# Optimization experiments

Measured on AMD Instinct MI355X. Metric: run time of the kernel, lower is better.

The kernel has to match this reference:

```python
import jax, jax.numpy as jnp
import numpy as np

BOHR = 1.8897261258369282  # au.BOHR length conversion constant


def setup_inputs() -> dict:
    key = jax.random.key(0)
    k0, k1, k2, k3, k4, k5, k6 = jax.random.split(key, 7)
    B, N, NK = 2, 4096, 4096
    coords = jax.random.normal(k0, (B, N, 3), jnp.float32) * 5.0
    q = jax.random.normal(k1, (B, N), jnp.float32)
    cell_inv = jax.random.normal(k2, (3, 3), jnp.float32) * 0.05  # inverse cell matrix
    kvec = jax.random.normal(k3, (NK, 3), jnp.float32)            # reciprocal lattice vectors
    expfac = jax.random.uniform(k4, (NK,), jnp.float32)           # exp(-k^2/4b^2)/k^2 factors
    volume = jax.random.uniform(k5, (1,), jnp.float32) + 100.0    # cell volume (positive)
    bewald = jax.random.uniform(k6, (1,), jnp.float32)            # Ewald splitting parameter
    return {"coords": coords, "q": q, "cell_inv": cell_inv, "kvec": kvec,
            "expfac": expfac, "volume": volume, "bewald": bewald}


def reference(coords, q, cell_inv, kvec, expfac, volume, bewald):
    # fractional coordinates: s[b,n,i] = cell_inv[i,j] coords[b,n,j]
    s = jnp.einsum('ij,bnj->bni', cell_inv, coords)
    # phase theta[b,n,k] = 2*pi * (kvec[k] . s[b,n]);  ks = i*theta in the original
    theta = (2.0 * jnp.pi) * jnp.einsum('kd,bnd->bnk', kvec, s)
    c = jnp.cos(theta)
    sn = jnp.sin(theta)
    # structure factor Sm[b,k] = sum_n q[b,n] * exp(i*theta[b,n,k])
    s_re = jnp.einsum('bn,bnk->bk', q, c)
    s_im = jnp.einsum('bn,bnk->bk', q, sn)
    # Re( expfac * Sm * exp(-i*theta) ) = expfac * (Sre*cos + Sim*sin)
    recip = (jnp.einsum('k,bk,bnk->bn', expfac, s_re, c)
             + jnp.einsum('k,bk,bnk->bn', expfac, s_im, sn))
    phi = recip * (BOHR / (jnp.pi * volume[0])) \
          - q * (2.0 * bewald[0] * BOHR / jnp.pi ** 0.5)
    return (0.5 * q * phi, phi)
```

## Files before the change

kernel.cpp:

```cpp
#include <hip/hip_runtime.h>


constexpr int B  = 2;
constexpr int N  = 4096;
constexpr int NK = 4096;
constexpr int TPB = 256;
constexpr int NSPLIT1 = 16;
constexpr int NSPLIT2 = 16;

constexpr int KT_OFF  = 0;
constexpr int SRE_OFF = NK * 3;
constexpr int SIM_OFF = SRE_OFF + B * NK;
constexpr int REC_OFF = SIM_OFF + B * NK;
constexpr int WS_FLOATS = REC_OFF + B * N;

__global__ __launch_bounds__(256) void prep_kt(const float* __restrict__ kvec,
                                               const float* __restrict__ cinv,
                                               float* __restrict__ ws) {
    int k = blockIdx.x * TPB + threadIdx.x;
    if (k >= NK) return;
    float k0 = kvec[k * 3 + 0], k1 = kvec[k * 3 + 1], k2 = kvec[k * 3 + 2];
    ws[KT_OFF + k * 3 + 0] = fmaf(k0, cinv[0], fmaf(k1, cinv[3], k2 * cinv[6]));
    ws[KT_OFF + k * 3 + 1] = fmaf(k0, cinv[1], fmaf(k1, cinv[4], k2 * cinv[7]));
    ws[KT_OFF + k * 3 + 2] = fmaf(k0, cinv[2], fmaf(k1, cinv[5], k2 * cinv[8]));
}

__global__ __launch_bounds__(256) void sf_kernel(const float* __restrict__ coords,
                                                 const float* __restrict__ q,
                                                 float* __restrict__ ws) {
    const int b = blockIdx.z;
    const int k = blockIdx.x * TPB + threadIdx.x;
    const int chunk = N / NSPLIT1;
    const int n0 = blockIdx.y * chunk;
    const float* cb = coords + (size_t)b * N * 3;
    const float* qb = q + (size_t)b * N;

    const float kt0 = ws[KT_OFF + k * 3 + 0];
    const float kt1 = ws[KT_OFF + k * 3 + 1];
    const float kt2 = ws[KT_OFF + k * 3 + 2];

    __shared__ float sc[TPB * 3];
    __shared__ float sq[TPB];

    float sre0 = 0.f, sre1 = 0.f, sim0 = 0.f, sim1 = 0.f;

    for (int t0 = 0; t0 < chunk; t0 += TPB) {
        const int base = n0 + t0;
        __syncthreads();
        sq[threadIdx.x] = qb[base + threadIdx.x];
#pragma unroll
        for (int j = 0; j < 3; ++j)
            sc[j * TPB + threadIdx.x] = cb[(size_t)base * 3 + j * TPB + threadIdx.x];
        __syncthreads();
#pragma unroll 8
        for (int i = 0; i < TPB; i += 2) {
            {
                float x = sc[3 * i + 0], y = sc[3 * i + 1], z = sc[3 * i + 2];
                float rev = fmaf(kt0, x, fmaf(kt1, y, kt2 * z));
                float r = rev - floorf(rev);
                float sn = __builtin_amdgcn_sinf(r);
                float cs = __builtin_amdgcn_cosf(r);
                float qv = sq[i];
                sre0 = fmaf(qv, cs, sre0);
                sim0 = fmaf(qv, sn, sim0);
            }
            {
                float x = sc[3 * i + 3], y = sc[3 * i + 4], z = sc[3 * i + 5];
                float rev = fmaf(kt0, x, fmaf(kt1, y, kt2 * z));
                float r = rev - floorf(rev);
                float sn = __builtin_amdgcn_sinf(r);
                float cs = __builtin_amdgcn_cosf(r);
                float qv = sq[i + 1];
                sre1 = fmaf(qv, cs, sre1);
                sim1 = fmaf(qv, sn, sim1);
            }
        }
    }
    atomicAdd(&ws[SRE_OFF + b * NK + k], sre0 + sre1);
    atomicAdd(&ws[SIM_OFF + b * NK + k], sim0 + sim1);
}

__global__ __launch_bounds__(256) void recip_kernel(const float* __restrict__ coords,
                                                    const float* __restrict__ expfac,
                                                    float* __restrict__ ws) {
    const int b = blockIdx.z;
    const int n = blockIdx.x * TPB + threadIdx.x;
    const int chunk = NK / NSPLIT2;
    const int k0 = blockIdx.y * chunk;

    const float* cp = coords + ((size_t)b * N + n) * 3;
    const float x = cp[0], y = cp[1], z = cp[2];

    __shared__ float skt[TPB * 3];
    __shared__ float sre[TPB];
    __shared__ float sim[TPB];

    float acc0 = 0.f, acc1 = 0.f;

    for (int t0 = 0; t0 < chunk; t0 += TPB) {
        const int kb = k0 + t0;
        const int t = threadIdx.x;
        __syncthreads();
        {
            float ef = expfac[kb + t];
            sre[t] = ef * ws[SRE_OFF + b * NK + kb + t];
            sim[t] = ef * ws[SIM_OFF + b * NK + kb + t];
#pragma unroll
            for (int j = 0; j < 3; ++j)
                skt[j * TPB + t] = ws[KT_OFF + (size_t)kb * 3 + j * TPB + t];
        }
        __syncthreads();
#pragma unroll 8
        for (int i = 0; i < TPB; i += 2) {
            {
                float kt0 = skt[3 * i + 0], kt1 = skt[3 * i + 1], kt2 = skt[3 * i + 2];
                float rev = fmaf(kt0, x, fmaf(kt1, y, kt2 * z));
                float r = rev - floorf(rev);
                float sn = __builtin_amdgcn_sinf(r);
                float cs = __builtin_amdgcn_cosf(r);
                acc0 = fmaf(sre[i], cs, fmaf(sim[i], sn, acc0));
            }
            {
                float kt0 = skt[3 * i + 3], kt1 = skt[3 * i + 4], kt2 = skt[3 * i + 5];
                float rev = fmaf(kt0, x, fmaf(kt1, y, kt2 * z));
                float r = rev - floorf(rev);
                float sn = __builtin_amdgcn_sinf(r);
                float cs = __builtin_amdgcn_cosf(r);
                acc1 = fmaf(sre[i + 1], cs, fmaf(sim[i + 1], sn, acc1));
            }
        }
    }
    atomicAdd(&ws[REC_OFF + b * N + n], acc0 + acc1);
}

__global__ __launch_bounds__(256) void final_kernel(const float* __restrict__ q,
                                                    const float* __restrict__ volume,
                                                    const float* __restrict__ bewald,
                                                    const float* __restrict__ ws,
                                                    float* __restrict__ out) {
    int i = blockIdx.x * TPB + threadIdx.x;
    if (i >= B * N) return;
    const float BOHRf = 1.8897261258369282f;
    const float PIf = 3.14159265358979323846f;
    const float inv_sqrt_pi = 0.5641895835477563f;
    float scale = BOHRf / (PIf * volume[0]);
    float self = 2.0f * bewald[0] * BOHRf * inv_sqrt_pi;
    float qv = q[i];
    float phi = ws[REC_OFF + i] * scale - qv * self;
    out[i] = 0.5f * qv * phi;
    out[B * N + i] = phi;
}

extern "C" void kernel_launch(void* const* d_in, const int* in_sizes, int n_in,
                              void* d_out, int out_size, void* d_ws, size_t ws_size,
                              hipStream_t stream) {
    const float* coords = (const float*)d_in[0];
    const float* q      = (const float*)d_in[1];
    const float* cinv   = (const float*)d_in[2];
    const float* kvec   = (const float*)d_in[3];
    const float* expfac = (const float*)d_in[4];
    const float* volume = (const float*)d_in[5];
    const float* bewald = (const float*)d_in[6];
    float* out = (float*)d_out;
    float* ws  = (float*)d_ws;

    hipMemsetAsync(ws + SRE_OFF, 0, (size_t)(WS_FLOATS - SRE_OFF) * sizeof(float), stream);

    prep_kt<<<dim3(NK / TPB), dim3(TPB), 0, stream>>>(kvec, cinv, ws);
    sf_kernel<<<dim3(NK / TPB, NSPLIT1, B), dim3(TPB), 0, stream>>>(coords, q, ws);
    recip_kernel<<<dim3(N / TPB, NSPLIT2, B), dim3(TPB), 0, stream>>>(coords, expfac, ws);
    final_kernel<<<dim3((B * N + TPB - 1) / TPB), dim3(TPB), 0, stream>>>(q, volume, bewald, ws, out);
}
```

Measured before the change: 93.22 us.

## Pack atoms and k-vectors as float4, pre-scale structure factors, split finer

```diff
diff --git a/kernel.cpp b/kernel.cpp
--- a/kernel.cpp
+++ b/kernel.cpp
@@ -1,136 +1,117 @@
 #include <hip/hip_runtime.h>
 
 
-constexpr int B  = 2;
-constexpr int N  = 4096;
-constexpr int NK = 4096;
+constexpr int B   = 2;
+constexpr int N   = 4096;
+constexpr int NK  = 4096;
 constexpr int TPB = 256;
-constexpr int NSPLIT1 = 16;
-constexpr int NSPLIT2 = 16;
+constexpr int NS1 = 64;
+constexpr int NS2 = 64;
+constexpr int TILE1 = N / NS1;
+constexpr int TILE2 = NK / NS2;
 
-constexpr int KT_OFF  = 0;
-constexpr int SRE_OFF = NK * 3;
-constexpr int SIM_OFF = SRE_OFF + B * NK;
-constexpr int REC_OFF = SIM_OFF + B * NK;
-constexpr int WS_FLOATS = REC_OFF + B * N;
+constexpr int KT4 = 0;
+constexpr int AT4 = KT4 + NK * 4;
+constexpr int SRE = AT4 + B * N * 4;
+constexpr int SIM = SRE + B * NK;
+constexpr int REC = SIM + B * NK;
+constexpr int SP  = REC + B * N;
+constexpr int ZERO_FLOATS = 2 * B * NK + B * N;
 
-__global__ __launch_bounds__(256) void prep_kt(const float* __restrict__ kvec,
-                                               const float* __restrict__ cinv,
-                                               float* __restrict__ ws) {
-    int k = blockIdx.x * TPB + threadIdx.x;
-    if (k >= NK) return;
-    float k0 = kvec[k * 3 + 0], k1 = kvec[k * 3 + 1], k2 = kvec[k * 3 + 2];
-    ws[KT_OFF + k * 3 + 0] = fmaf(k0, cinv[0], fmaf(k1, cinv[3], k2 * cinv[6]));
-    ws[KT_OFF + k * 3 + 1] = fmaf(k0, cinv[1], fmaf(k1, cinv[4], k2 * cinv[7]));
-    ws[KT_OFF + k * 3 + 2] = fmaf(k0, cinv[2], fmaf(k1, cinv[5], k2 * cinv[8]));
+__global__ __launch_bounds__(256) void prep_kernel(const float* __restrict__ coords,
+                                                   const float* __restrict__ q,
+                                                   const float* __restrict__ cinv,
+                                                   const float* __restrict__ kvec,
+                                                   float* __restrict__ ws) {
+    int i = blockIdx.x * TPB + threadIdx.x;
+    if (i < NK) {
+        float k0 = kvec[i * 3 + 0], k1 = kvec[i * 3 + 1], k2 = kvec[i * 3 + 2];
+        ws[KT4 + 4 * i + 0] = fmaf(k0, cinv[0], fmaf(k1, cinv[3], k2 * cinv[6]));
+        ws[KT4 + 4 * i + 1] = fmaf(k0, cinv[1], fmaf(k1, cinv[4], k2 * cinv[7]));
+        ws[KT4 + 4 * i + 2] = fmaf(k0, cinv[2], fmaf(k1, cinv[5], k2 * cinv[8]));
+        ws[KT4 + 4 * i + 3] = 0.f;
+    }
+    if (i < B * N) {
+        ws[AT4 + 4 * i + 0] = coords[3 * i + 0];
+        ws[AT4 + 4 * i + 1] = coords[3 * i + 1];
+        ws[AT4 + 4 * i + 2] = coords[3 * i + 2];
+        ws[AT4 + 4 * i + 3] = q[i];
+    }
 }
 
-__global__ __launch_bounds__(256) void sf_kernel(const float* __restrict__ coords,
-                                                 const float* __restrict__ q,
-                                                 float* __restrict__ ws) {
+__global__ __launch_bounds__(256) void sf_kernel(float* __restrict__ ws) {
     const int b = blockIdx.z;
     const int k = blockIdx.x * TPB + threadIdx.x;
-    const int chunk = N / NSPLIT1;
-    const int n0 = blockIdx.y * chunk;
-    const float* cb = coords + (size_t)b * N * 3;
-    const float* qb = q + (size_t)b * N;
+    const int n0 = blockIdx.y * TILE1;
 
-    const float kt0 = ws[KT_OFF + k * 3 + 0];
-    const float kt1 = ws[KT_OFF + k * 3 + 1];
-    const float kt2 = ws[KT_OFF + k * 3 + 2];
+    const float4 kt = *(const float4*)&ws[KT4 + 4 * k];
 
-    __shared__ float sc[TPB * 3];
-    __shared__ float sq[TPB];
+    __shared__ float sat[TILE1 * 4];
+    sat[threadIdx.x] = ws[AT4 + (size_t)(b * N + n0) * 4 + threadIdx.x];
+    __syncthreads();
 
+    const float4* a4 = (const float4*)sat;
     float sre0 = 0.f, sre1 = 0.f, sim0 = 0.f, sim1 = 0.f;
-
-    for (int t0 = 0; t0 < chunk; t0 += TPB) {
-        const int base = n0 + t0;
-        __syncthreads();
-        sq[threadIdx.x] = qb[base + threadIdx.x];
 #pragma unroll
-        for (int j = 0; j < 3; ++j)
-            sc[j * TPB + threadIdx.x] = cb[(size_t)base * 3 + j * TPB + threadIdx.x];
-        __syncthreads();
-#pragma unroll 8
-        for (int i = 0; i < TPB; i += 2) {
-            {
-                float x = sc[3 * i + 0], y = sc[3 * i + 1], z = sc[3 * i + 2];
-                float rev = fmaf(kt0, x, fmaf(kt1, y, kt2 * z));
-                float r = rev - floorf(rev);
-                float sn = __builtin_amdgcn_sinf(r);
-                float cs = __builtin_amdgcn_cosf(r);
-                float qv = sq[i];
-                sre0 = fmaf(qv, cs, sre0);
-                sim0 = fmaf(qv, sn, sim0);
-            }
-            {
-                float x = sc[3 * i + 3], y = sc[3 * i + 4], z = sc[3 * i + 5];
-                float rev = fmaf(kt0, x, fmaf(kt1, y, kt2 * z));
-                float r = rev - floorf(rev);
-                float sn = __builtin_amdgcn_sinf(r);
-                float cs = __builtin_amdgcn_cosf(r);
-                float qv = sq[i + 1];
-                sre1 = fmaf(qv, cs, sre1);
-                sim1 = fmaf(qv, sn, sim1);
-            }
-        }
+    for (int i = 0; i < TILE1; i += 2) {
+        float4 a = a4[i];
+        float4 c = a4[i + 1];
+        float r0 = fmaf(kt.x, a.x, fmaf(kt.y, a.y, kt.z * a.z));
+        r0 -= floorf(r0);
+        float r1 = fmaf(kt.x, c.x, fmaf(kt.y, c.y, kt.z * c.z));
+        r1 -= floorf(r1);
+        sre0 = fmaf(a.w, __builtin_amdgcn_cosf(r0), sre0);
+        sim0 = fmaf(a.w, __builtin_amdgcn_sinf(r0), sim0);
+        sre1 = fmaf(c.w, __builtin_amdgcn_cosf(r1), sre1);
+        sim1 = fmaf(c.w, __builtin_amdgcn_sinf(r1), sim1);
     }
-    atomicAdd(&ws[SRE_OFF + b * NK + k], sre0 + sre1);
-    atomicAdd(&ws[SIM_OFF + b * NK + k], sim0 + sim1);
+    atomicAdd(&ws[SRE + b * NK + k], sre0 + sre1);
+    atomicAdd(&ws[SIM + b * NK + k], sim0 + sim1);
 }
 
-__global__ __launch_bounds__(256) void recip_kernel(const float* __restrict__ coords,
-                                                    const float* __restrict__ expfac,
-                                                    float* __restrict__ ws) {
+__global__ __launch_bounds__(256) void pack_kernel(const float* __restrict__ expfac,
+                                                   float* __restrict__ ws) {
+    int i = blockIdx.x * TPB + threadIdx.x;
+    if (i >= B * NK) return;
+    int k = i & (NK - 1);
+    float ef = expfac[k];
+    ws[SP + 2 * i + 0] = ef * ws[SRE + i];
+    ws[SP + 2 * i + 1] = ef * ws[SIM + i];
+}
+
+__global__ __launch_bounds__(256) void recip_kernel(float* __restrict__ ws) {
     const int b = blockIdx.z;
     const int n = blockIdx.x * TPB + threadIdx.x;
-    const int chunk = NK / NSPLIT2;
-    const int k0 = blockIdx.y * chunk;
+    const int k0 = blockIdx.y * TILE2;
 
-    const float* cp = coords + ((size_t)b * N + n) * 3;
-    const float x = cp[0], y = cp[1], z = cp[2];
+    const float4 at = *(const float4*)&ws[AT4 + (size_t)(b * N + n) * 4];
 
-    __shared__ float skt[TPB * 3];
-    __shared__ float sre[TPB];
-    __shared__ float sim[TPB];
+    __shared__ float skt[TILE2 * 4];
+    __shared__ float ssp[TILE2 * 2];
+    skt[threadIdx.x] = ws[KT4 + k0 * 4 + threadIdx.x];
+    if (threadIdx.x < TILE2 * 2)
+        ssp[threadIdx.x] = ws[SP + (size_t)(b * NK + k0) * 2 + threadIdx.x];
+    __syncthreads();
 
+    const float4* kt4 = (const float4*)skt;
+    const float2* sp2 = (const float2*)ssp;
     float acc0 = 0.f, acc1 = 0.f;
-
-    for (int t0 = 0; t0 < chunk; t0 += TPB) {
-        const int kb = k0 + t0;
-        const int t = threadIdx.x;
-        __syncthreads();
-        {
-            float ef = expfac[kb + t];
-            sre[t] = ef * ws[SRE_OFF + b * NK + kb + t];
-            sim[t] = ef * ws[SIM_OFF + b * NK + kb + t];
 #pragma unroll
-            for (int j = 0; j < 3; ++j)
-                skt[j * TPB + t] = ws[KT_OFF + (size_t)kb * 3 + j * TPB + t];
-        }
-        __syncthreads();
-#pragma unroll 8
-        for (int i = 0; i < TPB; i += 2) {
-            {
-                float kt0 = skt[3 * i + 0], kt1 = skt[3 * i + 1], kt2 = skt[3 * i + 2];
-                float rev = fmaf(kt0, x, fmaf(kt1, y, kt2 * z));
-                float r = rev - floorf(rev);
-                float sn = __builtin_amdgcn_sinf(r);
-                float cs = __builtin_amdgcn_cosf(r);
-                acc0 = fmaf(sre[i], cs, fmaf(sim[i], sn, acc0));
-            }
-            {
-                float kt0 = skt[3 * i + 3], kt1 = skt[3 * i + 4], kt2 = skt[3 * i + 5];
-                float rev = fmaf(kt0, x, fmaf(kt1, y, kt2 * z));
-                float r = rev - floorf(rev);
-                float sn = __builtin_amdgcn_sinf(r);
-                float cs = __builtin_amdgcn_cosf(r);
-                acc1 = fmaf(sre[i + 1], cs, fmaf(sim[i + 1], sn, acc1));
-            }
-        }
+    for (int i = 0; i < TILE2; i += 2) {
+        float4 kt = kt4[i];
+        float2 sp = sp2[i];
+        float r0 = fmaf(kt.x, at.x, fmaf(kt.y, at.y, kt.z * at.z));
+        r0 -= floorf(r0);
+        acc0 = fmaf(sp.x, __builtin_amdgcn_cosf(r0),
+                    fmaf(sp.y, __builtin_amdgcn_sinf(r0), acc0));
+        float4 kt1 = kt4[i + 1];
+        float2 sp1 = sp2[i + 1];
+        float r1 = fmaf(kt1.x, at.x, fmaf(kt1.y, at.y, kt1.z * at.z));
+        r1 -= floorf(r1);
+        acc1 = fmaf(sp1.x, __builtin_amdgcn_cosf(r1),
+                    fmaf(sp1.y, __builtin_amdgcn_sinf(r1), acc1));
     }
-    atomicAdd(&ws[REC_OFF + b * N + n], acc0 + acc1);
+    atomicAdd(&ws[REC + b * N + n], acc0 + acc1);
 }
 
 __global__ __launch_bounds__(256) void final_kernel(const float* __restrict__ q,
@@ -146,7 +127,7 @@
     float scale = BOHRf / (PIf * volume[0]);
     float self = 2.0f * bewald[0] * BOHRf * inv_sqrt_pi;
     float qv = q[i];
-    float phi = ws[REC_OFF + i] * scale - qv * self;
+    float phi = ws[REC + i] * scale - qv * self;
     out[i] = 0.5f * qv * phi;
     out[B * N + i] = phi;
 }
@@ -164,10 +145,11 @@
     float* out = (float*)d_out;
     float* ws  = (float*)d_ws;
 
-    hipMemsetAsync(ws + SRE_OFF, 0, (size_t)(WS_FLOATS - SRE_OFF) * sizeof(float), stream);
+    hipMemsetAsync(ws + SRE, 0, (size_t)ZERO_FLOATS * sizeof(float), stream);
 
-    prep_kt<<<dim3(NK / TPB), dim3(TPB), 0, stream>>>(kvec, cinv, ws);
-    sf_kernel<<<dim3(NK / TPB, NSPLIT1, B), dim3(TPB), 0, stream>>>(coords, q, ws);
-    recip_kernel<<<dim3(N / TPB, NSPLIT2, B), dim3(TPB), 0, stream>>>(coords, expfac, ws);
-    final_kernel<<<dim3((B * N + TPB - 1) / TPB), dim3(TPB), 0, stream>>>(q, volume, bewald, ws, out);
+    prep_kernel<<<dim3((B * N) / TPB), dim3(TPB), 0, stream>>>(coords, q, cinv, kvec, ws);
+    sf_kernel<<<dim3(NK / TPB, NS1, B), dim3(TPB), 0, stream>>>(ws);
+    pack_kernel<<<dim3((B * NK) / TPB), dim3(TPB), 0, stream>>>(expfac, ws);
+    recip_kernel<<<dim3(N / TPB, NS2, B), dim3(TPB), 0, stream>>>(ws);
+    final_kernel<<<dim3((B * N) / TPB), dim3(TPB), 0, stream>>>(q, volume, bewald, ws, out);
 }
```

Result: no change. 93.68 us (+0.5%).
